# Kernel optimization log

Hardware: AMD Instinct MI355X
Metric: run time of the kernel (lower is better)

The kernel has to match this reference:

```python
import jax, jax.numpy as jnp
import numpy as np

N_NODES = 100000
N_EDGES = 150000
D_IN = 512
D_HID = 512
N_GRAPHS = 64


def setup_inputs() -> dict:
    key = jax.random.key(0)
    ks = jax.random.split(key, 12)
    x = jax.random.normal(ks[0], (N_NODES, D_IN), dtype=jnp.float32)
    edge_index = jax.random.randint(ks[1], (2, N_EDGES), 0, N_NODES, dtype=jnp.int64)
    batch = jnp.sort(jax.random.randint(ks[2], (N_NODES,), 0, N_GRAPHS, dtype=jnp.int64))
    s1 = 1.0 / np.sqrt(D_IN)
    s2 = 1.0 / np.sqrt(D_HID)
    # GINConv layer 1: MLP([D_IN, D_HID, D_HID])
    W1a = jax.random.uniform(ks[3], (D_IN, D_HID), jnp.float32, -s1, s1)
    b1a = jax.random.uniform(ks[4], (D_HID,), jnp.float32, -s1, s1)
    W1b = jax.random.uniform(ks[5], (D_HID, D_HID), jnp.float32, -s2, s2)
    b1b = jax.random.uniform(ks[6], (D_HID,), jnp.float32, -s2, s2)
    # GINConv layer 2 (out_channels=1): MLP([D_HID, 1, 1])
    W2a = jax.random.uniform(ks[7], (D_HID, 1), jnp.float32, -s2, s2)
    b2a = jax.random.uniform(ks[8], (1,), jnp.float32, -s2, s2)
    W2b = jax.random.uniform(ks[9], (1, 1), jnp.float32, -1.0, 1.0)
    b2b = jax.random.uniform(ks[10], (1,), jnp.float32, -1.0, 1.0)
    return {"x": x, "edge_index": edge_index, "batch": batch,
            "W1a": W1a, "b1a": b1a, "W1b": W1b, "b1b": b1b,
            "W2a": W2a, "b2a": b2a, "W2b": W2b, "b2b": b2b}


def _gin_conv(h, src, dst, Wa, ba, Wb, bb):
    # sum-aggregate neighbor features, add (1+eps)*x with eps=0, then MLP
    agg = jax.ops.segment_sum(h[src], dst, num_segments=N_NODES)  # [N, d]
    z = agg + h
    z = jnp.maximum(jnp.dot(z, Wa) + ba, 0.0)  # Linear -> ReLU
    return jnp.dot(z, Wb) + bb                  # Linear (plain last)


def reference(x, edge_index, batch, W1a, b1a, W1b, b1b, W2a, b2a, W2b, b2b):
    src, dst = edge_index[0], edge_index[1]
    h = _gin_conv(x, src, dst, W1a, b1a, W1b, b1b)
    h = jnp.maximum(h, 0.0)  # inter-layer activation (not applied after last layer)
    h = _gin_conv(h, src, dst, W2a, b2a, W2b, b2b)  # [N, 1]
    # global mean pool over graph assignment
    sums = jax.ops.segment_sum(h, batch, num_segments=N_GRAPHS)  # [G, 1]
    cnt = jax.ops.segment_sum(jnp.ones((N_NODES, 1), h.dtype), batch, num_segments=N_GRAPHS)
    return sums / jnp.maximum(cnt, 1.0)
```

## Files before the change

kernel.cpp:

```cpp
#include <hip/hip_runtime.h>
#include <hip/hip_bf16.h>

#define N_NODES_C 100000
#define N_EDGES_C 150000
#define DC 512
#define NG 64

typedef float f32x4 __attribute__((ext_vector_type(4)));
typedef short s16x8 __attribute__((ext_vector_type(8)));
typedef unsigned int u32;

__device__ __forceinline__ short f2bf(float f) {
    union { float f; unsigned u; } c; c.f = f;
    unsigned r = c.u + 0x7fffu + ((c.u >> 16) & 1u);
    return (short)(r >> 16);
}
__device__ __forceinline__ float bf2f(short v) {
    union { unsigned u; float f; } c;
    c.u = ((unsigned)(unsigned short)v) << 16;
    return c.f;
}

__device__ __forceinline__ void gload16(const void* g, void* l) {
    __builtin_amdgcn_global_load_lds((const __attribute__((address_space(1))) u32*)g,
                                     (__attribute__((address_space(3))) u32*)l,
                                     16, 0, 0);
}


__global__ void zero_k(float* s, float* aggs, int* cnt, float* gsum, float* gcnt) {
    int i = blockIdx.x * 256 + threadIdx.x;
    if (i < N_NODES_C) { s[i] = 0.f; aggs[i] = 0.f; cnt[i] = 0; }
    if (i < NG) { gsum[i] = 0.f; gcnt[i] = 0.f; }
}

__global__ void cvt_k(const float* __restrict__ x, short* __restrict__ xb, int n8) {
    int i = blockIdx.x * 256 + threadIdx.x;
    int stride = gridDim.x * 256;
    const f32x4* xs = (const f32x4*)x;
    s16x8* o = (s16x8*)xb;
    for (; i < n8; i += stride) {
        f32x4 a = xs[i * 2];
        f32x4 b = xs[i * 2 + 1];
        s16x8 r;
        r[0] = f2bf(a.x); r[1] = f2bf(a.y); r[2] = f2bf(a.z); r[3] = f2bf(a.w);
        r[4] = f2bf(b.x); r[5] = f2bf(b.y); r[6] = f2bf(b.z); r[7] = f2bf(b.w);
        o[i] = r;
    }
}

__global__ void transpose_w(const float* __restrict__ in, short* __restrict__ out) {
    __shared__ float tile[32][33];
    int tx = threadIdx.x & 31;
    int ty = threadIdx.x >> 5;
    int k0 = blockIdx.y * 32;
    int n0 = blockIdx.x * 32;
#pragma unroll
    for (int i = 0; i < 4; ++i)
        tile[ty + i * 8][tx] = in[(size_t)(k0 + ty + i * 8) * DC + n0 + tx];
    __syncthreads();
#pragma unroll
    for (int i = 0; i < 4; ++i)
        out[(size_t)(n0 + ty + i * 8) * DC + k0 + tx] = f2bf(tile[tx][ty + i * 8]);
}


__global__ void hist_k(const int* __restrict__ ei, int* __restrict__ cnt) {
    int e = blockIdx.x * 256 + threadIdx.x;
    if (e < N_EDGES_C) atomicAdd(&cnt[ei[N_EDGES_C + e]], 1);
}

__global__ void scan1_k(const int* __restrict__ cnt, int* __restrict__ off,
                        int* __restrict__ bsum) {
    __shared__ int sh[1024];
    int tid = threadIdx.x;
    int i = blockIdx.x * 1024 + tid;
    int v = (i < N_NODES_C) ? cnt[i] : 0;
    sh[tid] = v;
    __syncthreads();
    for (int d = 1; d < 1024; d <<= 1) {
        int t = (tid >= d) ? sh[tid - d] : 0;
        __syncthreads();
        sh[tid] += t;
        __syncthreads();
    }
    if (i < N_NODES_C) off[i] = sh[tid] - v;
    if (tid == 1023) bsum[blockIdx.x] = sh[1023];
}

#define NSCAN_BLK 98

__global__ void scan2_k(int* __restrict__ bsum) {
    __shared__ int sh[128];
    int tid = threadIdx.x;
    int v = (tid < NSCAN_BLK) ? bsum[tid] : 0;
    sh[tid] = v;
    __syncthreads();
    for (int d = 1; d < 128; d <<= 1) {
        int t = (tid >= d) ? sh[tid - d] : 0;
        __syncthreads();
        sh[tid] += t;
        __syncthreads();
    }
    if (tid < NSCAN_BLK) bsum[tid] = sh[tid] - v;
}

__global__ void scan3_k(int* __restrict__ off, const int* __restrict__ bsum) {
    int i = blockIdx.x * 1024 + threadIdx.x;
    if (i < N_NODES_C) off[i] += bsum[blockIdx.x];
}

__global__ void place_k(const int* __restrict__ ei, int* __restrict__ off,
                        int* __restrict__ ssrc) {
    int e = blockIdx.x * 256 + threadIdx.x;
    if (e < N_EDGES_C) {
        int d = ei[N_EDGES_C + e];
        int p = atomicAdd(&off[d], 1);
        ssrc[p] = ei[e];
    }
}

__global__ void gather_relu_k(const short* __restrict__ y, const int* __restrict__ off,
                              const int* __restrict__ ssrc, const float* __restrict__ b1a,
                              short* __restrict__ z1) {
    int node = blockIdx.x * 4 + (threadIdx.x >> 6);
    if (node >= N_NODES_C) return;
    int t = threadIdx.x & 63;
    const int col = t * 8;
    int beg = (node == 0) ? 0 : off[node - 1];
    int end = off[node];
    s16x8 own = *(const s16x8*)(y + (size_t)node * DC + col);
    float acc[8];
#pragma unroll
    for (int q = 0; q < 8; ++q) acc[q] = bf2f(own[q]);
    int j = beg;
    for (; j + 2 <= end; j += 2) {
        int s0 = ssrc[j];
        int s1 = ssrc[j + 1];
        s16x8 r0 = *(const s16x8*)(y + (size_t)s0 * DC + col);
        s16x8 r1 = *(const s16x8*)(y + (size_t)s1 * DC + col);
#pragma unroll
        for (int q = 0; q < 8; ++q) acc[q] += bf2f(r0[q]) + bf2f(r1[q]);
    }
    if (j < end) {
        int s0 = ssrc[j];
        s16x8 r0 = *(const s16x8*)(y + (size_t)s0 * DC + col);
#pragma unroll
        for (int q = 0; q < 8; ++q) acc[q] += bf2f(r0[q]);
    }
    f32x4 bv0 = *(const f32x4*)(b1a + col);
    f32x4 bv1 = *(const f32x4*)(b1a + col + 4);
    s16x8 o;
    o[0] = f2bf(fmaxf(acc[0] + bv0.x, 0.f));
    o[1] = f2bf(fmaxf(acc[1] + bv0.y, 0.f));
    o[2] = f2bf(fmaxf(acc[2] + bv0.z, 0.f));
    o[3] = f2bf(fmaxf(acc[3] + bv0.w, 0.f));
    o[4] = f2bf(fmaxf(acc[4] + bv1.x, 0.f));
    o[5] = f2bf(fmaxf(acc[5] + bv1.y, 0.f));
    o[6] = f2bf(fmaxf(acc[6] + bv1.z, 0.f));
    o[7] = f2bf(fmaxf(acc[7] + bv1.w, 0.f));
    *(s16x8*)(z1 + (size_t)node * DC + col) = o;
}


__global__ void edge_scalar(const int* __restrict__ ei, const float* __restrict__ s,
                            float* __restrict__ aggs) {
    int e = blockIdx.x * 256 + threadIdx.x;
    if (e < N_EDGES_C) atomicAdd(&aggs[ei[N_EDGES_C + e]], s[ei[e]]);
}

__global__ void node_pool(const float* __restrict__ s, const float* __restrict__ aggs,
                          const int* __restrict__ batch, const float* __restrict__ b2a,
                          float* __restrict__ gsum, float* __restrict__ gcnt) {
    __shared__ float ls[NG], lc[NG];
    int t = threadIdx.x;
    if (t < NG) { ls[t] = 0.f; lc[t] = 0.f; }
    __syncthreads();
    int i = blockIdx.x * 256 + t;
    if (i < N_NODES_C) {
        float z2 = fmaxf(aggs[i] + s[i] + b2a[0], 0.0f);
        int g = batch[i];
        atomicAdd(&ls[g], z2);
        atomicAdd(&lc[g], 1.0f);
    }
    __syncthreads();
    if (t < NG && lc[t] != 0.f) {
        atomicAdd(&gsum[t], ls[t]);
        atomicAdd(&gcnt[t], lc[t]);
    }
}

__global__ void finalize_k(const float* gsum, const float* gcnt, const float* w2b,
                           const float* b2b, float* out) {
    int g = threadIdx.x;
    if (g < NG) {
        float c = fmaxf(gcnt[g], 1.0f);
        out[g] = gsum[g] / c * w2b[0] + b2b[0];
    }
}

#define BM 128
#define BN 128
#define BK 32
#define NRB 782
#define NCB 4
#define NWG (NRB * NCB)
#define WG_PER_XCD (NWG / 8)

template <int EPI>
__global__ __launch_bounds__(256, 2) void gemm_k(const short* __restrict__ A,
                                                 const short* __restrict__ Bt,
                                                 const float* __restrict__ bias,
                                                 short* __restrict__ Cout,
                                                 const float* __restrict__ w2a,
                                                 float* __restrict__ s_out) {
    __shared__ alignas(16) short As[BM * BK];
    __shared__ alignas(16) short Bs[BN * BK];

    const int tid = threadIdx.x;
    const int bid = blockIdx.x;
    const int lin = (bid & 7) * WG_PER_XCD + (bid >> 3);
    const int brow = (lin >> 2) * BM;
    const int bcol = (lin & 3) * BN;

    const int w    = tid >> 6;
    const int lane = tid & 63;
    const int wr   = (w >> 1) * 64;
    const int wc   = (w & 1) * 64;
    const int lr   = lane & 15;
    const int lk   = (lane >> 4) * 8;

    f32x4 acc[4][4] = {};

    const int srow = lane >> 2;
    const int scol = (lane & 3) * 8;
    int ar0 = brow + w * 32 + srow;
    int ar1 = ar0 + 16;
    if (ar0 >= N_NODES_C) ar0 = N_NODES_C - 1;
    if (ar1 >= N_NODES_C) ar1 = N_NODES_C - 1;
    const short* ag0 = A + (size_t)ar0 * DC + scol;
    const short* ag1 = A + (size_t)ar1 * DC + scol;
    const short* bg0 = Bt + (size_t)(bcol + w * 32 + srow) * DC + scol;
    const short* bg1 = bg0 + (size_t)16 * DC;
    short* al0 = &As[(w * 32) * BK];
    short* al1 = &As[(w * 32 + 16) * BK];
    short* bl0 = &Bs[(w * 32) * BK];
    short* bl1 = &Bs[(w * 32 + 16) * BK];

    for (int kt = 0; kt < DC / BK; ++kt) {
        const int k0 = kt * BK;
        __syncthreads();
        gload16(ag0 + k0, al0);
        gload16(ag1 + k0, al1);
        gload16(bg0 + k0, bl0);
        gload16(bg1 + k0, bl1);
        __syncthreads();

        s16x8 af[4], bfr[4];
#pragma unroll
        for (int mi = 0; mi < 4; ++mi)
            af[mi] = *(const s16x8*)&As[(wr + mi * 16 + lr) * BK + lk];
#pragma unroll
        for (int ni = 0; ni < 4; ++ni)
            bfr[ni] = *(const s16x8*)&Bs[(wc + ni * 16 + lr) * BK + lk];
#pragma unroll
        for (int mi = 0; mi < 4; ++mi)
#pragma unroll
            for (int ni = 0; ni < 4; ++ni)
                acc[mi][ni] = __builtin_amdgcn_mfma_f32_16x16x32_bf16(af[mi], bfr[ni],
                                                                      acc[mi][ni], 0, 0, 0);
    }

    const int rb = brow + wr + (lane >> 4) * 4;
    const int cb = bcol + wc + lr;

    if constexpr (EPI == 2) {
#pragma unroll
        for (int mi = 0; mi < 4; ++mi) {
#pragma unroll
            for (int r = 0; r < 4; ++r) {
                int row = rb + mi * 16 + r;
                if (row < N_NODES_C) {
#pragma unroll
                    for (int ni = 0; ni < 4; ++ni)
                        Cout[(size_t)row * DC + cb + ni * 16] = f2bf(acc[mi][ni][r]);
                }
            }
        }
    } else {
        float bv[4], wv[4];
#pragma unroll
        for (int ni = 0; ni < 4; ++ni) {
            bv[ni] = bias[cb + ni * 16];
            wv[ni] = w2a[cb + ni * 16];
        }
#pragma unroll
        for (int mi = 0; mi < 4; ++mi) {
#pragma unroll
            for (int r = 0; r < 4; ++r) {
                float sum = 0.f;
#pragma unroll
                for (int ni = 0; ni < 4; ++ni) {
                    float v = fmaxf(acc[mi][ni][r] + bv[ni], 0.0f);
                    sum += v * wv[ni];
                }
#pragma unroll
                for (int off = 1; off < 16; off <<= 1) sum += __shfl_xor(sum, off, 64);
                int row = rb + mi * 16 + r;
                if (lr == 0 && row < N_NODES_C) atomicAdd(&s_out[row], sum);
            }
        }
    }
}


extern "C" void kernel_launch(void* const* d_in, const int* in_sizes, int n_in,
                              void* d_out, int out_size, void* d_ws, size_t ws_size,
                              hipStream_t stream) {
    const float* x     = (const float*)d_in[0];
    const int*   ei    = (const int*)d_in[1];
    const int*   batch = (const int*)d_in[2];
    const float* W1a   = (const float*)d_in[3];
    const float* b1a   = (const float*)d_in[4];
    const float* W1b   = (const float*)d_in[5];
    const float* b1b   = (const float*)d_in[6];
    const float* W2a   = (const float*)d_in[7];
    const float* b2a   = (const float*)d_in[8];
    const float* W2b   = (const float*)d_in[9];
    const float* b2b   = (const float*)d_in[10];
    float* out = (float*)d_out;

    char* w = (char*)d_ws;
    short* buf0 = (short*)(w);
    short* y    = (short*)(w + 102400000);
    short* WT1  = (short*)(w + 204800000);
    short* WT2  = (short*)(w + 205324288);
    float* sbuf = (float*)(w + 205848576);
    float* aggs = (float*)(w + 206248576);
    int*   cnt  = (int*)  (w + 206648576);
    int*   offb = (int*)  (w + 207048576);
    int*   ssrc = (int*)  (w + 207448576);
    int*   bsum = (int*)  (w + 208048576);
    float* gsum = (float*)(w + 208049088);
    float* gcnt = (float*)(w + 208049344);

    zero_k<<<391, 256, 0, stream>>>(sbuf, aggs, cnt, gsum, gcnt);
    transpose_w<<<dim3(16, 16), 256, 0, stream>>>(W1a, WT1);
    transpose_w<<<dim3(16, 16), 256, 0, stream>>>(W1b, WT2);

    cvt_k<<<2048, 256, 0, stream>>>(x, buf0, N_NODES_C * DC / 8);

    hist_k<<<586, 256, 0, stream>>>(ei, cnt);
    scan1_k<<<NSCAN_BLK, 1024, 0, stream>>>(cnt, offb, bsum);
    scan2_k<<<1, 128, 0, stream>>>(bsum);
    scan3_k<<<NSCAN_BLK, 1024, 0, stream>>>(offb, bsum);
    place_k<<<586, 256, 0, stream>>>(ei, offb, ssrc);

    gemm_k<2><<<NWG, 256, 0, stream>>>(buf0, WT1, nullptr, y, nullptr, nullptr);
    gather_relu_k<<<25000, 256, 0, stream>>>(y, offb, ssrc, b1a, buf0);
    gemm_k<1><<<NWG, 256, 0, stream>>>(buf0, WT2, b1b, nullptr, W2a, sbuf);

    edge_scalar<<<586, 256, 0, stream>>>(ei, sbuf, aggs);
    node_pool<<<391, 256, 0, stream>>>(sbuf, aggs, batch, b2a, gsum, gcnt);
    finalize_k<<<1, 64, 0, stream>>>(gsum, gcnt, W2b, b2b, out);
}
```

Before: 312.4 us.

## Double-buffer GEMM LDS tiles with async prefetch two stages ahead

Converts the single-buffered GEMM k-loop into a double-buffered pipeline. The global-to-LDS loads for tile kt+2 are issued while tile kt+1 is still in flight, and hand-written s_waitcnt vmcnt and s_barrier instructions replace the two __syncthreads per iteration. This is meant to hide global load latency behind the MFMA work. It doubles LDS use per workgroup, which could limit occupancy, and it depends on manual wait-count correctness.

```diff
diff --git a/kernel.cpp b/kernel.cpp
--- a/kernel.cpp
+++ b/kernel.cpp
@@ -202,10 +202,16 @@
 #define BM 128
 #define BN 128
 #define BK 32
+#define NKT (DC / BK)
 #define NRB 782
 #define NCB 4
 #define NWG (NRB * NCB)
 #define WG_PER_XCD (NWG / 8)
+
+#define BARRIER() asm volatile("s_barrier" ::: "memory")
+#define WAIT_VM4() asm volatile("s_waitcnt vmcnt(4)" ::: "memory")
+#define WAIT_VM0() asm volatile("s_waitcnt vmcnt(0)" ::: "memory")
+#define WAIT_LGKM0() asm volatile("s_waitcnt lgkmcnt(0)" ::: "memory")
 
 template <int EPI>
 __global__ __launch_bounds__(256, 2) void gemm_k(const short* __restrict__ A,
@@ -214,8 +220,8 @@
                                                  short* __restrict__ Cout,
                                                  const float* __restrict__ w2a,
                                                  float* __restrict__ s_out) {
-    __shared__ alignas(16) short As[BM * BK];
-    __shared__ alignas(16) short Bs[BN * BK];
+    __shared__ alignas(16) short As[2][BM * BK];
+    __shared__ alignas(16) short Bs[2][BN * BK];
 
     const int tid = threadIdx.x;
     const int bid = blockIdx.x;
@@ -242,34 +248,51 @@
     const short* ag1 = A + (size_t)ar1 * DC + scol;
     const short* bg0 = Bt + (size_t)(bcol + w * 32 + srow) * DC + scol;
     const short* bg1 = bg0 + (size_t)16 * DC;
-    short* al0 = &As[(w * 32) * BK];
-    short* al1 = &As[(w * 32 + 16) * BK];
-    short* bl0 = &Bs[(w * 32) * BK];
-    short* bl1 = &Bs[(w * 32 + 16) * BK];
-
-    for (int kt = 0; kt < DC / BK; ++kt) {
-        const int k0 = kt * BK;
-        __syncthreads();
-        gload16(ag0 + k0, al0);
-        gload16(ag1 + k0, al1);
-        gload16(bg0 + k0, bl0);
-        gload16(bg1 + k0, bl1);
-        __syncthreads();
-
+
+#define STAGE(t, buf)                                          \
+    do {                                                       \
+        gload16(ag0 + (t) * BK, &As[buf][(w * 32) * BK]);      \
+        gload16(ag1 + (t) * BK, &As[buf][(w * 32 + 16) * BK]); \
+        gload16(bg0 + (t) * BK, &Bs[buf][(w * 32) * BK]);      \
+        gload16(bg1 + (t) * BK, &Bs[buf][(w * 32 + 16) * BK]); \
+    } while (0)
+
+    STAGE(0, 0);
+    STAGE(1, 1);
+    WAIT_VM4();
+    __builtin_amdgcn_sched_barrier(0);
+    BARRIER();
+
+#pragma unroll
+    for (int kt = 0; kt < NKT; ++kt) {
+        const int cur = kt & 1;
         s16x8 af[4], bfr[4];
 #pragma unroll
         for (int mi = 0; mi < 4; ++mi)
-            af[mi] = *(const s16x8*)&As[(wr + mi * 16 + lr) * BK + lk];
+            af[mi] = *(const s16x8*)&As[cur][(wr + mi * 16 + lr) * BK + lk];
 #pragma unroll
         for (int ni = 0; ni < 4; ++ni)
-            bfr[ni] = *(const s16x8*)&Bs[(wc + ni * 16 + lr) * BK + lk];
+            bfr[ni] = *(const s16x8*)&Bs[cur][(wc + ni * 16 + lr) * BK + lk];
 #pragma unroll
         for (int mi = 0; mi < 4; ++mi)
 #pragma unroll
             for (int ni = 0; ni < 4; ++ni)
                 acc[mi][ni] = __builtin_amdgcn_mfma_f32_16x16x32_bf16(af[mi], bfr[ni],
                                                                       acc[mi][ni], 0, 0, 0);
-    }
+        if (kt == NKT - 1) break;
+
+        WAIT_LGKM0();
+        BARRIER();
+        if (kt + 2 < NKT) {
+            STAGE(kt + 2, cur);
+            WAIT_VM4();
+        } else {
+            WAIT_VM0();
+        }
+        __builtin_amdgcn_sched_barrier(0);
+        BARRIER();
+    }
+#undef STAGE
 
     const int rb = brow + wr + (lane >> 4) * 4;
     const int cb = bcol + wc + lr;
```

New measurement: 309.7 us, median of 2. About the same (-0.9%).

## Fuse fp32-to-bf16 conversion of x into first GEMM A-tile load

Applied to the files above, without the earlier changes.

Removes the standalone cvt_k pass. The first GEMM now reads fp32 x directly, converting to bf16 in registers with a one-tile register prefetch, then writes the tile to LDS. This drops a full write and read of the 100MB bf16 copy. It also raises launch bounds to 3 waves-per-SIMD occupancy and adds s_setprio around the MFMA block. The trade-off is that each GEMM reads 4 row-blocks of fp32 A (twice the bytes of bf16), does conversion ALU work per column block, and the higher occupancy target may pressure registers.

```diff
diff --git a/kernel.cpp b/kernel.cpp
--- a/kernel.cpp
+++ b/kernel.cpp
@@ -32,21 +32,6 @@
     int i = blockIdx.x * 256 + threadIdx.x;
     if (i < N_NODES_C) { s[i] = 0.f; aggs[i] = 0.f; cnt[i] = 0; }
     if (i < NG) { gsum[i] = 0.f; gcnt[i] = 0.f; }
-}
-
-__global__ void cvt_k(const float* __restrict__ x, short* __restrict__ xb, int n8) {
-    int i = blockIdx.x * 256 + threadIdx.x;
-    int stride = gridDim.x * 256;
-    const f32x4* xs = (const f32x4*)x;
-    s16x8* o = (s16x8*)xb;
-    for (; i < n8; i += stride) {
-        f32x4 a = xs[i * 2];
-        f32x4 b = xs[i * 2 + 1];
-        s16x8 r;
-        r[0] = f2bf(a.x); r[1] = f2bf(a.y); r[2] = f2bf(a.z); r[3] = f2bf(a.w);
-        r[4] = f2bf(b.x); r[5] = f2bf(b.y); r[6] = f2bf(b.z); r[7] = f2bf(b.w);
-        o[i] = r;
-    }
 }
 
 __global__ void transpose_w(const float* __restrict__ in, short* __restrict__ out) {
@@ -202,13 +187,14 @@
 #define BM 128
 #define BN 128
 #define BK 32
+#define NKT (DC / BK)
 #define NRB 782
 #define NCB 4
 #define NWG (NRB * NCB)
 #define WG_PER_XCD (NWG / 8)
 
-template <int EPI>
-__global__ __launch_bounds__(256, 2) void gemm_k(const short* __restrict__ A,
+template <int ASRC, int EPI>
+__global__ __launch_bounds__(256, 3) void gemm_k(const void* __restrict__ Ap,
                                                  const short* __restrict__ Bt,
                                                  const float* __restrict__ bias,
                                                  short* __restrict__ Cout,
@@ -234,28 +220,68 @@
 
     const int srow = lane >> 2;
     const int scol = (lane & 3) * 8;
-    int ar0 = brow + w * 32 + srow;
-    int ar1 = ar0 + 16;
-    if (ar0 >= N_NODES_C) ar0 = N_NODES_C - 1;
-    if (ar1 >= N_NODES_C) ar1 = N_NODES_C - 1;
-    const short* ag0 = A + (size_t)ar0 * DC + scol;
-    const short* ag1 = A + (size_t)ar1 * DC + scol;
     const short* bg0 = Bt + (size_t)(bcol + w * 32 + srow) * DC + scol;
     const short* bg1 = bg0 + (size_t)16 * DC;
-    short* al0 = &As[(w * 32) * BK];
-    short* al1 = &As[(w * 32 + 16) * BK];
     short* bl0 = &Bs[(w * 32) * BK];
     short* bl1 = &Bs[(w * 32 + 16) * BK];
 
-    for (int kt = 0; kt < DC / BK; ++kt) {
+    const short* ag0 = nullptr;
+    const short* ag1 = nullptr;
+    short* al0 = nullptr;
+    short* al1 = nullptr;
+    const float* af32 = nullptr;
+    f32x4 areg[4];
+    const int awrow = tid >> 1;
+    const int awcol = (tid & 1) * 16;
+
+    if constexpr (ASRC == 1) {
+        int ar0 = brow + w * 32 + srow;
+        int ar1 = ar0 + 16;
+        if (ar0 >= N_NODES_C) ar0 = N_NODES_C - 1;
+        if (ar1 >= N_NODES_C) ar1 = N_NODES_C - 1;
+        ag0 = (const short*)Ap + (size_t)ar0 * DC + scol;
+        ag1 = (const short*)Ap + (size_t)ar1 * DC + scol;
+        al0 = &As[(w * 32) * BK];
+        al1 = &As[(w * 32 + 16) * BK];
+    } else {
+        int ar = brow + awrow;
+        if (ar >= N_NODES_C) ar = N_NODES_C - 1;
+        af32 = (const float*)Ap + (size_t)ar * DC + awcol;
+#pragma unroll
+        for (int q = 0; q < 4; ++q) areg[q] = *(const f32x4*)(af32 + q * 4);
+    }
+
+    for (int kt = 0; kt < NKT; ++kt) {
         const int k0 = kt * BK;
         __syncthreads();
-        gload16(ag0 + k0, al0);
-        gload16(ag1 + k0, al1);
+        if constexpr (ASRC == 1) {
+            gload16(ag0 + k0, al0);
+            gload16(ag1 + k0, al1);
+        } else {
+            s16x8 c0, c1;
+            c0[0] = f2bf(areg[0].x); c0[1] = f2bf(areg[0].y);
+            c0[2] = f2bf(areg[0].z); c0[3] = f2bf(areg[0].w);
+            c0[4] = f2bf(areg[1].x); c0[5] = f2bf(areg[1].y);
+            c0[6] = f2bf(areg[1].z); c0[7] = f2bf(areg[1].w);
+            c1[0] = f2bf(areg[2].x); c1[1] = f2bf(areg[2].y);
+            c1[2] = f2bf(areg[2].z); c1[3] = f2bf(areg[2].w);
+            c1[4] = f2bf(areg[3].x); c1[5] = f2bf(areg[3].y);
+            c1[6] = f2bf(areg[3].z); c1[7] = f2bf(areg[3].w);
+            *(s16x8*)&As[awrow * BK + awcol + 0] = c0;
+            *(s16x8*)&As[awrow * BK + awcol + 8] = c1;
+        }
         gload16(bg0 + k0, bl0);
         gload16(bg1 + k0, bl1);
         __syncthreads();
 
+        if constexpr (ASRC == 0) {
+            if (kt + 1 < NKT) {
+#pragma unroll
+                for (int q = 0; q < 4; ++q)
+                    areg[q] = *(const f32x4*)(af32 + (kt + 1) * BK + q * 4);
+            }
+        }
+
         s16x8 af[4], bfr[4];
 #pragma unroll
         for (int mi = 0; mi < 4; ++mi)
@@ -263,12 +289,14 @@
 #pragma unroll
         for (int ni = 0; ni < 4; ++ni)
             bfr[ni] = *(const s16x8*)&Bs[(wc + ni * 16 + lr) * BK + lk];
+        __builtin_amdgcn_s_setprio(1);
 #pragma unroll
         for (int mi = 0; mi < 4; ++mi)
 #pragma unroll
             for (int ni = 0; ni < 4; ++ni)
                 acc[mi][ni] = __builtin_amdgcn_mfma_f32_16x16x32_bf16(af[mi], bfr[ni],
                                                                       acc[mi][ni], 0, 0, 0);
+        __builtin_amdgcn_s_setprio(0);
     }
 
     const int rb = brow + wr + (lane >> 4) * 4;
@@ -331,7 +359,7 @@
     float* out = (float*)d_out;
 
     char* w = (char*)d_ws;
-    short* buf0 = (short*)(w);
+    short* z1   = (short*)(w);
     short* y    = (short*)(w + 102400000);
     short* WT1  = (short*)(w + 204800000);
     short* WT2  = (short*)(w + 205324288);
@@ -348,17 +376,15 @@
     transpose_w<<<dim3(16, 16), 256, 0, stream>>>(W1a, WT1);
     transpose_w<<<dim3(16, 16), 256, 0, stream>>>(W1b, WT2);
 
-    cvt_k<<<2048, 256, 0, stream>>>(x, buf0, N_NODES_C * DC / 8);
-
     hist_k<<<586, 256, 0, stream>>>(ei, cnt);
     scan1_k<<<NSCAN_BLK, 1024, 0, stream>>>(cnt, offb, bsum);
     scan2_k<<<1, 128, 0, stream>>>(bsum);
     scan3_k<<<NSCAN_BLK, 1024, 0, stream>>>(offb, bsum);
     place_k<<<586, 256, 0, stream>>>(ei, offb, ssrc);
 
-    gemm_k<2><<<NWG, 256, 0, stream>>>(buf0, WT1, nullptr, y, nullptr, nullptr);
-    gather_relu_k<<<25000, 256, 0, stream>>>(y, offb, ssrc, b1a, buf0);
-    gemm_k<1><<<NWG, 256, 0, stream>>>(buf0, WT2, b1b, nullptr, W2a, sbuf);
+    gemm_k<0, 2><<<NWG, 256, 0, stream>>>(x, WT1, nullptr, y, nullptr, nullptr);
+    gather_relu_k<<<25000, 256, 0, stream>>>(y, offb, ssrc, b1a, z1);
+    gemm_k<1, 1><<<NWG, 256, 0, stream>>>(z1, WT2, b1b, nullptr, W2a, sbuf);
 
     edge_scalar<<<586, 256, 0, stream>>>(ei, sbuf, aggs);
     node_pool<<<391, 256, 0, stream>>>(sbuf, aggs, batch, b2a, gsum, gcnt);
```

Result: faster. 297.4 us (-4.8%).
